# Kernel optimization log

Hardware: AMD Instinct MI355X
Metric: run time of the kernel (lower is better)

The kernel has to match this reference:

```python
import jax, jax.numpy as jnp
import numpy as np

EPS = 1e-5
TEMP = 0.07
LARGE_NEG = -1e9


def mi_net(x, W1, g1, b1, W2, b2, Ws, lng, lnb):
    # x: (B, C, T). 1x1 convs == per-position channel projections.
    y = jnp.einsum('bct,oc->bot', x, W1)                      # conv1 (no bias)
    mu = y.mean(axis=(0, 2), keepdims=True)                   # BatchNorm2d, training-mode batch stats
    var = y.var(axis=(0, 2), keepdims=True)
    y = (y - mu) * jax.lax.rsqrt(var + EPS) * g1[None, :, None] + b1[None, :, None]
    y = jax.nn.relu(y)
    y = jnp.einsum('bot,po->bpt', y, W2) + b2[None, :, None]  # conv2 (bias)
    h = y + jnp.einsum('bct,oc->bot', x, Ws)                  # linear shortcut
    mu2 = h.mean(axis=1, keepdims=True)                       # LayerNorm over channel dim
    v2 = h.var(axis=1, keepdims=True)
    return (h - mu2) * jax.lax.rsqrt(v2 + EPS) * lng[None, :, None] + lnb[None, :, None]


def infonce(L, G):
    # L: (N, D, T) locals, G: (N, D) single global per sample (n_multis = 1)
    N, D, T = L.shape
    l_p = jnp.swapaxes(L, 1, 2)                               # (N, T, D)
    l_p = l_p / jnp.linalg.norm(l_p, axis=2, keepdims=True)
    g = G / jnp.linalg.norm(G, axis=1, keepdims=True)         # (N, D)
    u_p = (jnp.einsum('ntd,nd->nt', l_p, g) / TEMP)[:, :, None]   # (N, T, 1), positives scaled by temp
    # negatives: <global_i, local_{j,t}>; NOT divided by temperature (faithful to torch source)
    u_n = jnp.einsum('nd,mtd->nmt', g, l_p)                   # (N, N, T)
    eye = jnp.eye(N, dtype=bool)[:, :, None]
    u_n = jnp.where(eye, LARGE_NEG, u_n).reshape(N, N * T)    # mask self pairs
    logits = jnp.concatenate(
        [u_p, jnp.broadcast_to(u_n[:, None, :], (N, T, N * T))], axis=2)  # (N, T, 1+N*T)
    logp = jax.nn.log_softmax(logits, axis=2)
    return -logp[:, :, 0].mean()


def setup_inputs() -> dict:
    key = jax.random.key(0)
    ks = jax.random.split(key, 10)
    B, CL, CG, T, MI = 32, 1536, 192, 256, 512
    d = {
        'local_feat': jax.random.normal(ks[0], (B, CL, T), jnp.float32),
        'global_feat': jax.random.normal(ks[1], (B, CG), jnp.float32),
        # local_net params
        'lW1': jax.random.normal(ks[2], (MI, CL), jnp.float32) * 0.02,
        'lg1': jnp.ones((MI,), jnp.float32),
        'lb1': jnp.zeros((MI,), jnp.float32),
        'lW2': jax.random.normal(ks[3], (MI, MI), jnp.float32) * 0.02,
        'lb2': jnp.zeros((MI,), jnp.float32),
        'lWs': jax.random.normal(ks[4], (MI, CL), jnp.float32) * 0.02,
        'llng': jnp.ones((MI,), jnp.float32),
        'llnb': jnp.zeros((MI,), jnp.float32),
        # global_net params (global_channels != mi_units -> net exists)
        'gW1': jax.random.normal(ks[5], (MI, CG), jnp.float32) * 0.02,
        'gg1': jnp.ones((MI,), jnp.float32),
        'gb1': jnp.zeros((MI,), jnp.float32),
        'gW2': jax.random.normal(ks[6], (MI, MI), jnp.float32) * 0.02,
        'gb2': jnp.zeros((MI,), jnp.float32),
    }
    # shortcut with near-identity init (n_units >= n_input for global net)
    gWs = jax.random.uniform(ks[7], (MI, CG), jnp.float32, -0.01, 0.01)
    gWs = gWs.at[jnp.arange(CG), jnp.arange(CG)].set(1.0)
    d['gWs'] = gWs
    d['glng'] = jnp.ones((MI,), jnp.float32)
    d['glnb'] = jnp.zeros((MI,), jnp.float32)
    return d


def reference(local_feat, global_feat,
              lW1, lg1, lb1, lW2, lb2, lWs, llng, llnb,
              gW1, gg1, gb1, gW2, gb2, gWs, glng, glnb):
    L = mi_net(local_feat, lW1, lg1, lb1, lW2, lb2, lWs, llng, llnb)      # (B, MI, T)
    G = mi_net(global_feat[:, :, None], gW1, gg1, gb1, gW2, gb2, gWs, glng, glnb)[:, :, 0]  # (B, MI)
    return infonce(L, G)
```

## Files before the change

kernel.cpp:

```cpp
#include <hip/hip_runtime.h>

#define B 32
#define CL 1536
#define CG 192
#define T 256
#define MI 512
#define NPOS 8192
#define EPS 1e-5f
#define TEMP 0.07f

typedef __attribute__((ext_vector_type(8))) __bf16 bf16x8;
typedef __attribute__((ext_vector_type(4))) float f32x4;

__device__ __forceinline__ unsigned short f2bf(float f) {
  union { float f; unsigned u; } v; v.f = f;
  unsigned r = v.u + 0x7FFFu + ((v.u >> 16) & 1u);
  return (unsigned short)(r >> 16);
}
__device__ __forceinline__ float bf2f(unsigned short h) {
  union { unsigned u; float f; } v; v.u = ((unsigned)h) << 16;
  return v.f;
}

__device__ __forceinline__ float wave_sum(float v) {
#pragma unroll
  for (int off = 32; off > 0; off >>= 1) v += __shfl_xor(v, off, 64);
  return v;
}
__device__ __forceinline__ float block_sum(float v, float* rb) {
  v = wave_sum(v);
  __syncthreads();
  if ((threadIdx.x & 63) == 0) rb[threadIdx.x >> 6] = v;
  __syncthreads();
  return rb[0] + rb[1] + rb[2] + rb[3];
}
__device__ __forceinline__ float bs128(float v, float* rb) {
  v = wave_sum(v);
  __syncthreads();
  if ((threadIdx.x & 63) == 0) rb[threadIdx.x >> 6] = v;
  __syncthreads();
  return rb[0] + rb[1];
}

__global__ __launch_bounds__(256) void k_prep(
    const float* __restrict__ x, const float* __restrict__ lW1,
    const float* __restrict__ lWs, const float* __restrict__ lW2,
    const float* __restrict__ gx, const float* __restrict__ gW1,
    unsigned short* __restrict__ xT, unsigned short* __restrict__ Wc,
    unsigned short* __restrict__ W2b, float* __restrict__ y1g,
    float* __restrict__ bsum) {
  __shared__ float xs[64][65];
  const int bi = blockIdx.x, tid = threadIdx.x;
  if (bi < 1792) {
    int idx = (bi * 256 + tid) * 4;
    const float* src; unsigned short* dst;
    if (idx < 786432) { src = lW1 + idx; dst = Wc + idx; }
    else if (idx < 1572864) { src = lWs + (idx - 786432); dst = Wc + idx; }
    else { src = lW2 + (idx - 1572864); dst = W2b + (idx - 1572864); }
    float4 v = *(const float4*)src;
    ushort4 o = {f2bf(v.x), f2bf(v.y), f2bf(v.z), f2bf(v.w)};
    *(ushort4*)dst = o;
  } else if (bi < 4864) {
    int bi2 = bi - 1792;
    int b = bi2 / 96, rem = bi2 - b * 96;
    int c0 = (rem >> 2) * 64, t0 = (rem & 3) * 64;
    const float* xb = x + ((size_t)b * CL + c0) * T + t0;
#pragma unroll
    for (int i = 0; i < 16; i++) {
      int idx = tid + i * 256, c = idx >> 6, t = idx & 63;
      xs[c][t] = xb[(size_t)c * T + t];
    }
    __syncthreads();
    unsigned short* ob = xT + ((size_t)b * T + t0) * CL + c0;
#pragma unroll
    for (int i = 0; i < 8; i++) {
      int idx = tid + i * 256, t = idx >> 5, k = (idx & 31) * 2;
      ushort2 v = {f2bf(xs[k][t]), f2bf(xs[k + 1][t])};
      *(ushort2*)&ob[(size_t)t * CL + k] = v;
    }
  } else if (bi < 4928) {
    int idx = (bi - 4864) * 256 + tid;
    int b = idx & 31, o = idx >> 5;
    float s = 0.f;
    for (int c = 0; c < CG; c++) s = fmaf(gx[b * CG + c], gW1[o * CG + c], s);
    y1g[o * 32 + b] = s;
  } else {
    float4 z = {0.f, 0.f, 0.f, 0.f};
    ((float4*)bsum)[tid] = z;
  }
}

__global__ __launch_bounds__(128, 4) void k_gemm1(
    const unsigned short* __restrict__ xT, const unsigned short* __restrict__ Wc,
    unsigned short* __restrict__ y1u, unsigned short* __restrict__ ysb,
    float* __restrict__ bsum, float* __restrict__ bsq,
    const float* __restrict__ y1g, const float* __restrict__ gg1,
    const float* __restrict__ gb1, const float* __restrict__ gW2,
    const float* __restrict__ gb2, const float* __restrict__ gx,
    const float* __restrict__ gWsc, float* __restrict__ hg) {
  const int tid = threadIdx.x, bi = blockIdx.x;
  if (bi >= 2048) {
    __shared__ float gsc[512], gsh[512];
#pragma unroll
    for (int jj = 0; jj < 4; jj++) {
      int o = tid + jj * 128;
      float s = 0.f, s2 = 0.f;
      for (int b = 0; b < 32; b++) {
        float v = y1g[o * 32 + b];
        s += v; s2 = fmaf(v, v, s2);
      }
      float mu = s * (1.f / 32.f);
      float var = s2 * (1.f / 32.f) - mu * mu;
      float sc = gg1[o] * rsqrtf(var + EPS);
      gsc[o] = sc;
      gsh[o] = gb1[o] - mu * sc;
    }
    __syncthreads();
    int base = (bi - 2048) * 256;
#pragma unroll
    for (int jj = 0; jj < 2; jj++) {
      int idx = base + jj * 128 + tid;
      int b = idx & 31, p = idx >> 5;
      float s = gb2[p];
      for (int o = 0; o < MI; o++) {
        float v = fmaxf(fmaf(y1g[o * 32 + b], gsc[o], gsh[o]), 0.f);
        s = fmaf(v, gW2[(size_t)p * MI + o], s);
      }
      for (int c = 0; c < CG; c++) s = fmaf(gx[b * CG + c], gWsc[p * CG + c], s);
      hg[p * 32 + b] = s;
    }
    return;
  }
  __shared__ __align__(16) unsigned short As[64][32];
  __shared__ __align__(16) unsigned short Bs[64][32];
  __shared__ float ps[64], pq[64];
  const int w = tid >> 6, lane = tid & 63;
  const int m0 = (bi & 127) * 64, o0 = (bi >> 7) * 64;
  const int sr = lane >> 2, sc = (lane & 3) * 8;
  const int lm = lane & 15, q = lane >> 4;
  f32x4 acc[4][2];
#pragma unroll
  for (int i = 0; i < 4; i++)
#pragma unroll
    for (int j = 0; j < 2; j++) acc[i][j] = f32x4{0.f, 0.f, 0.f, 0.f};

  const unsigned short* pa = xT + (size_t)(m0 + w * 32 + sr) * CL + sc;
  const unsigned short* pb = Wc + (size_t)(o0 + w * 32 + sr) * CL + sc;
  for (int k0 = 0; k0 < CL; k0 += 32) {
    __builtin_amdgcn_global_load_lds(
        (const __attribute__((address_space(1))) void*)(pa + k0),
        (__attribute__((address_space(3))) void*)&As[w * 32][0], 16, 0, 0);
    __builtin_amdgcn_global_load_lds(
        (const __attribute__((address_space(1))) void*)(pa + 16 * CL + k0),
        (__attribute__((address_space(3))) void*)&As[w * 32 + 16][0], 16, 0, 0);
    __builtin_amdgcn_global_load_lds(
        (const __attribute__((address_space(1))) void*)(pb + k0),
        (__attribute__((address_space(3))) void*)&Bs[w * 32][0], 16, 0, 0);
    __builtin_amdgcn_global_load_lds(
        (const __attribute__((address_space(1))) void*)(pb + 16 * CL + k0),
        (__attribute__((address_space(3))) void*)&Bs[w * 32 + 16][0], 16, 0, 0);
    __syncthreads();
    bf16x8 af[4], bfr[2];
#pragma unroll
    for (int mi = 0; mi < 4; mi++)
      af[mi] = *(const bf16x8*)&As[mi * 16 + lm][q * 8];
#pragma unroll
    for (int ni = 0; ni < 2; ni++)
      bfr[ni] = *(const bf16x8*)&Bs[w * 32 + ni * 16 + lm][q * 8];
#pragma unroll
    for (int mi = 0; mi < 4; mi++)
#pragma unroll
      for (int ni = 0; ni < 2; ni++)
        acc[mi][ni] = __builtin_amdgcn_mfma_f32_16x16x32_bf16(
            af[mi], bfr[ni], acc[mi][ni], 0, 0, 0);
    __syncthreads();
  }
  const int row0 = m0 + q * 4;
  const bool isY1 = (o0 < 512);
  unsigned short* dst = isY1 ? y1u : ysb;
  const int ob = isY1 ? o0 : o0 - 512;
#pragma unroll
  for (int mi = 0; mi < 4; mi++)
#pragma unroll
    for (int ni = 0; ni < 2; ni++) {
      int oc = ob + w * 32 + ni * 16 + lm;
#pragma unroll
      for (int r = 0; r < 4; r++)
        dst[(size_t)(row0 + mi * 16 + r) * 512 + oc] = f2bf(acc[mi][ni][r]);
    }
  if (isY1) {
#pragma unroll
    for (int ni = 0; ni < 2; ni++) {
      float s = 0.f, s2 = 0.f;
#pragma unroll
      for (int mi = 0; mi < 4; mi++)
#pragma unroll
        for (int r = 0; r < 4; r++) {
          float v = acc[mi][ni][r];
          s += v; s2 = fmaf(v, v, s2);
        }
      s += __shfl_xor(s, 16, 64);  s2 += __shfl_xor(s2, 16, 64);
      s += __shfl_xor(s, 32, 64);  s2 += __shfl_xor(s2, 32, 64);
      if (q == 0) {
        int c = w * 32 + ni * 16 + lm;
        ps[c] = s; pq[c] = s2;
      }
    }
    __syncthreads();
    if (tid < 64) {
      atomicAdd(&bsum[o0 + tid], ps[tid]);
      atomicAdd(&bsq[o0 + tid], pq[tid]);
    }
  }
}

__global__ __launch_bounds__(256) void k_bnapp(
    const unsigned short* __restrict__ y1u, const float* __restrict__ bsum,
    const float* __restrict__ bsq, const float* __restrict__ lg1,
    const float* __restrict__ lb1, unsigned short* __restrict__ vv) {
  int idx = (blockIdx.x * 256 + threadIdx.x) * 4;
  int o = idx & 511;
  ushort4 in = *(const ushort4*)&y1u[idx];
  float iv[4] = {bf2f(in.x), bf2f(in.y), bf2f(in.z), bf2f(in.w)};
  unsigned short ov[4];
#pragma unroll
  for (int j = 0; j < 4; j++) {
    float mu = bsum[o + j] * (1.f / NPOS);
    float var = bsq[o + j] * (1.f / NPOS) - mu * mu;
    float sc = lg1[o + j] * rsqrtf(var + EPS);
    float sh = lb1[o + j] - mu * sc;
    ov[j] = f2bf(fmaxf(fmaf(iv[j], sc, sh), 0.f));
  }
  ushort4 out = {ov[0], ov[1], ov[2], ov[3]};
  *(ushort4*)&vv[idx] = out;
}

__global__ __launch_bounds__(128, 4) void k_gemm2(
    const unsigned short* __restrict__ vv, const unsigned short* __restrict__ W2b,
    const float* __restrict__ b2, const unsigned short* __restrict__ ysb,
    unsigned short* __restrict__ hb16,
    const float* __restrict__ hg, const float* __restrict__ glng,
    const float* __restrict__ glnb, unsigned short* __restrict__ gnormb) {
  __shared__ __align__(16) unsigned short As[64][32];
  __shared__ __align__(16) unsigned short Bs[64][32];
  __shared__ float rb[2];
  const int tid = threadIdx.x, bi = blockIdx.x;
  if (bi >= 1024) {
    int b = bi - 1024;
    float v[4], Lv[4];
    float s = 0.f, s2 = 0.f;
#pragma unroll
    for (int j = 0; j < 4; j++) {
      v[j] = hg[(tid + j * 128) * 32 + b];
      s += v[j]; s2 = fmaf(v[j], v[j], s2);
    }
    s = bs128(s, rb);
    s2 = bs128(s2, rb);
    float mu = s * (1.f / MI);
    float var = s2 * (1.f / MI) - mu * mu;
    float rstd = rsqrtf(var + EPS);
    float n2 = 0.f;
#pragma unroll
    for (int j = 0; j < 4; j++) {
      int p = tid + j * 128;
      Lv[j] = fmaf((v[j] - mu) * rstd, glng[p], glnb[p]);
      n2 = fmaf(Lv[j], Lv[j], n2);
    }
    n2 = bs128(n2, rb);
    float inv = rsqrtf(n2);
#pragma unroll
    for (int j = 0; j < 4; j++)
      gnormb[b * MI + tid + j * 128] = f2bf(Lv[j] * inv);
    return;
  }
  const int w = tid >> 6, lane = tid & 63;
  const int m0 = (bi & 127) * 64, p0 = (bi >> 7) * 64;
  const int sr = lane >> 2, sc = (lane & 3) * 8;
  const int lm = lane & 15, q = lane >> 4;
  f32x4 acc[4][2];
#pragma unroll
  for (int i = 0; i < 4; i++)
#pragma unroll
    for (int j = 0; j < 2; j++) acc[i][j] = f32x4{0.f, 0.f, 0.f, 0.f};

  const unsigned short* pa = vv + (size_t)(m0 + w * 32 + sr) * 512 + sc;
  const unsigned short* pb = W2b + (size_t)(p0 + w * 32 + sr) * 512 + sc;
  for (int k0 = 0; k0 < 512; k0 += 32) {
    __builtin_amdgcn_global_load_lds(
        (const __attribute__((address_space(1))) void*)(pa + k0),
        (__attribute__((address_space(3))) void*)&As[w * 32][0], 16, 0, 0);
    __builtin_amdgcn_global_load_lds(
        (const __attribute__((address_space(1))) void*)(pa + 16 * 512 + k0),
        (__attribute__((address_space(3))) void*)&As[w * 32 + 16][0], 16, 0, 0);
    __builtin_amdgcn_global_load_lds(
        (const __attribute__((address_space(1))) void*)(pb + k0),
        (__attribute__((address_space(3))) void*)&Bs[w * 32][0], 16, 0, 0);
    __builtin_amdgcn_global_load_lds(
        (const __attribute__((address_space(1))) void*)(pb + 16 * 512 + k0),
        (__attribute__((address_space(3))) void*)&Bs[w * 32 + 16][0], 16, 0, 0);
    __syncthreads();
    bf16x8 af[4], bfr[2];
#pragma unroll
    for (int mi = 0; mi < 4; mi++)
      af[mi] = *(const bf16x8*)&As[mi * 16 + lm][q * 8];
#pragma unroll
    for (int ni = 0; ni < 2; ni++)
      bfr[ni] = *(const bf16x8*)&Bs[w * 32 + ni * 16 + lm][q * 8];
#pragma unroll
    for (int mi = 0; mi < 4; mi++)
#pragma unroll
      for (int ni = 0; ni < 2; ni++)
        acc[mi][ni] = __builtin_amdgcn_mfma_f32_16x16x32_bf16(
            af[mi], bfr[ni], acc[mi][ni], 0, 0, 0);
    __syncthreads();
  }
  const int row0 = m0 + q * 4;
#pragma unroll
  for (int ni = 0; ni < 2; ni++) {
    int p = p0 + w * 32 + ni * 16 + lm;
    float bias = b2[p];
#pragma unroll
    for (int mi = 0; mi < 4; mi++)
#pragma unroll
      for (int r = 0; r < 4; r++) {
        size_t off = (size_t)(row0 + mi * 16 + r) * 512 + p;
        hb16[off] = f2bf(acc[mi][ni][r] + bias + bf2f(ysb[off]));
      }
  }
}

__global__ __launch_bounds__(256) void k_tail(
    const unsigned short* __restrict__ hb16, const float* __restrict__ lng,
    const float* __restrict__ lnb, const unsigned short* __restrict__ gnormb,
    float* __restrict__ up, float* __restrict__ pmax, float* __restrict__ psum) {
  __shared__ __align__(16) unsigned short gs[32 * 512];
  __shared__ __align__(16) unsigned short Ls[32 * 512];
  __shared__ float Ured[4 * 1024];
  const int tid = threadIdx.x;
  const int w = tid >> 6, lane = tid & 63;
  const int r0 = blockIdx.x * 32;
  const int smp = r0 >> 8;
#pragma unroll
  for (int i = 0; i < 8; i++) {
    int e = (tid + i * 256) * 8;
    *(uint4*)&gs[e] = *(const uint4*)&gnormb[e];
  }
  float4 g0 = *(const float4*)&lng[lane * 8];
  float4 g1 = *(const float4*)&lng[lane * 8 + 4];
  float4 bb0 = *(const float4*)&lnb[lane * 8];
  float4 bb1 = *(const float4*)&lnb[lane * 8 + 4];
  float gg[8] = {g0.x, g0.y, g0.z, g0.w, g1.x, g1.y, g1.z, g1.w};
  float bz[8] = {bb0.x, bb0.y, bb0.z, bb0.w, bb1.x, bb1.y, bb1.z, bb1.w};
#pragma unroll
  for (int j = 0; j < 8; j++) {
    int rr = w * 8 + j;
    const unsigned short* row = hb16 + (size_t)(r0 + rr) * 512 + lane * 8;
    ushort4 u0 = *(const ushort4*)row;
    ushort4 u1 = *(const ushort4*)(row + 4);
    float v[8] = {bf2f(u0.x), bf2f(u0.y), bf2f(u0.z), bf2f(u0.w),
                  bf2f(u1.x), bf2f(u1.y), bf2f(u1.z), bf2f(u1.w)};
    float s = 0.f, s2 = 0.f;
#pragma unroll
    for (int k = 0; k < 8; k++) { s += v[k]; s2 = fmaf(v[k], v[k], s2); }
    s = wave_sum(s);
    s2 = wave_sum(s2);
    float mu = s * (1.f / MI);
    float var = s2 * (1.f / MI) - mu * mu;
    float rstd = rsqrtf(var + EPS);
    float L[8], n2 = 0.f;
#pragma unroll
    for (int k = 0; k < 8; k++) {
      L[k] = fmaf((v[k] - mu) * rstd, gg[k], bz[k]);
      n2 = fmaf(L[k], L[k], n2);
    }
    n2 = wave_sum(n2);
    float inv = rsqrtf(n2);
    unsigned short* orow = &Ls[rr * 512 + lane * 8];
    ushort4 o0 = {f2bf(L[0] * inv), f2bf(L[1] * inv), f2bf(L[2] * inv), f2bf(L[3] * inv)};
    ushort4 o1 = {f2bf(L[4] * inv), f2bf(L[5] * inv), f2bf(L[6] * inv), f2bf(L[7] * inv)};
    *(ushort4*)orow = o0;
    *(ushort4*)(orow + 4) = o1;
  }
  __syncthreads();
  const int lm = lane & 15, q = lane >> 4;
  f32x4 acc[2][2];
#pragma unroll
  for (int i = 0; i < 2; i++)
#pragma unroll
    for (int j = 0; j < 2; j++) acc[i][j] = f32x4{0.f, 0.f, 0.f, 0.f};
#pragma unroll
  for (int kk = 0; kk < 4; kk++) {
    int k0 = w * 128 + kk * 32 + q * 8;
    bf16x8 af[2], bfr[2];
#pragma unroll
    for (int mi = 0; mi < 2; mi++)
      af[mi] = *(const bf16x8*)&gs[(mi * 16 + lm) * 512 + k0];
#pragma unroll
    for (int ni = 0; ni < 2; ni++)
      bfr[ni] = *(const bf16x8*)&Ls[(ni * 16 + lm) * 512 + k0];
#pragma unroll
    for (int mi = 0; mi < 2; mi++)
#pragma unroll
      for (int ni = 0; ni < 2; ni++)
        acc[mi][ni] = __builtin_amdgcn_mfma_f32_16x16x32_bf16(
            af[mi], bfr[ni], acc[mi][ni], 0, 0, 0);
  }
#pragma unroll
  for (int mi = 0; mi < 2; mi++)
#pragma unroll
    for (int ni = 0; ni < 2; ni++)
#pragma unroll
      for (int r = 0; r < 4; r++) {
        int m = mi * 16 + q * 4 + r, n = ni * 16 + lm;
        Ured[w * 1024 + m * 32 + n] = acc[mi][ni][r];
      }
  __syncthreads();
  float u[4];
#pragma unroll
  for (int j = 0; j < 4; j++) {
    int idx = tid * 4 + j;
    u[j] = Ured[idx] + Ured[1024 + idx] + Ured[2048 + idx] + Ured[3072 + idx];
  }
  __syncthreads();
#pragma unroll
  for (int j = 0; j < 4; j++) Ured[tid * 4 + j] = u[j];
  int m = (tid * 4) >> 5;
  if (m == smp) {
#pragma unroll
    for (int j = 0; j < 4; j++)
      up[r0 + ((tid * 4 + j) & 31)] = u[j] * (1.f / TEMP);
  }
  __syncthreads();
  if (tid < 32) {
    float mx = -1e30f, s = 0.f;
    if (tid != smp) {
      for (int n = 0; n < 32; n++) mx = fmaxf(mx, Ured[tid * 32 + n]);
      for (int n = 0; n < 32; n++) s += expf(Ured[tid * 32 + n] - mx);
    }
    pmax[tid * 256 + blockIdx.x] = mx;
    psum[tid * 256 + blockIdx.x] = s;
  }
}

__global__ __launch_bounds__(256) void k_loss(
    const float* __restrict__ up, const float* __restrict__ pmax,
    const float* __restrict__ psum, float* __restrict__ out) {
  __shared__ float rb[4];
  __shared__ float red[32][8];
  __shared__ float Ms[32], Ss[32];
  const int tid = threadIdx.x;
  const int n = tid >> 3, j = tid & 7;
  float mx = -1e30f;
  for (int c = j * 32; c < j * 32 + 32; c++) mx = fmaxf(mx, pmax[n * 256 + c]);
  red[n][j] = mx;
  __syncthreads();
  if (j == 0) {
    float M = -1e30f;
#pragma unroll
    for (int k = 0; k < 8; k++) M = fmaxf(M, red[n][k]);
    Ms[n] = M;
  }
  __syncthreads();
  float M = Ms[n];
  float s = 0.f;
  for (int c = j * 32; c < j * 32 + 32; c++)
    s += psum[n * 256 + c] * expf(pmax[n * 256 + c] - M);
  __syncthreads();
  red[n][j] = s;
  __syncthreads();
  if (j == 0) {
    float S = 0.f;
#pragma unroll
    for (int k = 0; k < 8; k++) S += red[n][k];
    Ss[n] = S;
  }
  __syncthreads();
  float acc = 0.f;
  for (int i = tid; i < NPOS; i += 256) {
    int nn = i >> 8;
    float upv = up[i];
    float Mn = Ms[nn], Sn = Ss[nn];
    float mx2 = fmaxf(upv, Mn);
    float lse = mx2 + logf(expf(upv - mx2) + Sn * expf(Mn - mx2));
    acc += lse - upv;
  }
  acc = block_sum(acc, rb);
  if (tid == 0) out[0] = acc * (1.f / NPOS);
}

extern "C" void kernel_launch(void* const* d_in, const int* in_sizes, int n_in,
                              void* d_out, int out_size, void* d_ws, size_t ws_size,
                              hipStream_t stream) {
  (void)in_sizes; (void)n_in; (void)out_size; (void)ws_size;
  const float* x    = (const float*)d_in[0];
  const float* gx   = (const float*)d_in[1];
  const float* lW1  = (const float*)d_in[2];
  const float* lg1  = (const float*)d_in[3];
  const float* lb1  = (const float*)d_in[4];
  const float* lW2  = (const float*)d_in[5];
  const float* lb2  = (const float*)d_in[6];
  const float* lWs  = (const float*)d_in[7];
  const float* llng = (const float*)d_in[8];
  const float* llnb = (const float*)d_in[9];
  const float* gW1  = (const float*)d_in[10];
  const float* gg1  = (const float*)d_in[11];
  const float* gb1  = (const float*)d_in[12];
  const float* gW2  = (const float*)d_in[13];
  const float* gb2  = (const float*)d_in[14];
  const float* gWs  = (const float*)d_in[15];
  const float* glng = (const float*)d_in[16];
  const float* glnb = (const float*)d_in[17];

  char* wsb = (char*)d_ws;
  unsigned short* xT     = (unsigned short*)(wsb);
  unsigned short* Wc     = (unsigned short*)(wsb + 25165824);
  unsigned short* W2b    = (unsigned short*)(wsb + 28311552);
  unsigned short* y1u    = (unsigned short*)(wsb + 28835840);
  unsigned short* ysb    = (unsigned short*)(wsb + 37224448);
  unsigned short* vv     = (unsigned short*)(wsb + 45613056);
  unsigned short* hb16   = (unsigned short*)(wsb + 54001664);
  float* bsum            = (float*)(wsb + 71827456);
  float* bsq             = (float*)(wsb + 71829504);
  float* y1g             = (float*)(wsb + 71831552);
  float* hg              = (float*)(wsb + 71901184);
  unsigned short* gnormb = (unsigned short*)(wsb + 71966720);
  float* up              = (float*)(wsb + 71999488);
  float* pmax            = (float*)(wsb + 72032256);
  float* psum            = (float*)(wsb + 72065024);

  k_prep<<<dim3(4929), 256, 0, stream>>>(x, lW1, lWs, lW2, gx, gW1, xT, Wc, W2b,
                                         y1g, bsum);
  k_gemm1<<<dim3(2112), 128, 0, stream>>>(xT, Wc, y1u, ysb, bsum, bsq,
                                          y1g, gg1, gb1, gW2, gb2, gx, gWs, hg);
  k_bnapp<<<dim3(4096), 256, 0, stream>>>(y1u, bsum, bsq, lg1, lb1, vv);
  k_gemm2<<<dim3(1056), 128, 0, stream>>>(vv, W2b, lb2, ysb, hb16,
                                          hg, glng, glnb, gnormb);
  k_tail<<<dim3(256), 256, 0, stream>>>(hb16, llng, llnb, gnormb, up, pmax, psum);
  k_loss<<<dim3(1), 256, 0, stream>>>(up, pmax, psum, (float*)d_out);
}
```

Measured before the change: 254.2 us.

## Enlarge GEMM tiles to 128x128, move shortcut add into tail, relocate global LN

Both bf16 MFMA GEMMs go from 64x64 tiles with 128 threads to 128x128 tiles with 256 threads laid out as a 2x2 wave grid. This doubles operand reuse per LDS load and cuts global traffic, at the cost of far fewer blocks (256 for gemm2) and more accumulator registers. The shortcut add (ysb) moves from the gemm2 epilogue into k_tail, and the global-feature LayerNorm moves from gemm2 into k_bnapp. The x transpose in k_prep now writes 16-byte packed stores, and BN stat atomics are issued directly from each wave instead of going through shared memory.

```diff
diff --git a/kernel.cpp b/kernel.cpp
--- a/kernel.cpp
+++ b/kernel.cpp
@@ -33,13 +33,6 @@
   if ((threadIdx.x & 63) == 0) rb[threadIdx.x >> 6] = v;
   __syncthreads();
   return rb[0] + rb[1] + rb[2] + rb[3];
-}
-__device__ __forceinline__ float bs128(float v, float* rb) {
-  v = wave_sum(v);
-  __syncthreads();
-  if ((threadIdx.x & 63) == 0) rb[threadIdx.x >> 6] = v;
-  __syncthreads();
-  return rb[0] + rb[1];
 }
 
 __global__ __launch_bounds__(256) void k_prep(
@@ -73,10 +66,17 @@
     __syncthreads();
     unsigned short* ob = xT + ((size_t)b * T + t0) * CL + c0;
 #pragma unroll
-    for (int i = 0; i < 8; i++) {
-      int idx = tid + i * 256, t = idx >> 5, k = (idx & 31) * 2;
-      ushort2 v = {f2bf(xs[k][t]), f2bf(xs[k + 1][t])};
-      *(ushort2*)&ob[(size_t)t * CL + k] = v;
+    for (int half = 0; half < 2; half++) {
+      int s = tid + half * 256;
+      int t = s >> 3, kg = s & 7;
+      unsigned short v[8];
+#pragma unroll
+      for (int j = 0; j < 8; j++) v[j] = f2bf(xs[kg * 8 + j][t]);
+      uint4 o = {(unsigned)v[0] | ((unsigned)v[1] << 16),
+                 (unsigned)v[2] | ((unsigned)v[3] << 16),
+                 (unsigned)v[4] | ((unsigned)v[5] << 16),
+                 (unsigned)v[6] | ((unsigned)v[7] << 16)};
+      *(uint4*)&ob[(size_t)t * CL + kg * 8] = o;
     }
   } else if (bi < 4928) {
     int idx = (bi - 4864) * 256 + tid;
@@ -90,7 +90,7 @@
   }
 }
 
-__global__ __launch_bounds__(128, 4) void k_gemm1(
+__global__ __launch_bounds__(256, 2) void k_gemm1(
     const unsigned short* __restrict__ xT, const unsigned short* __restrict__ Wc,
     unsigned short* __restrict__ y1u, unsigned short* __restrict__ ysb,
     float* __restrict__ bsum, float* __restrict__ bsq,
@@ -99,11 +99,11 @@
     const float* __restrict__ gb2, const float* __restrict__ gx,
     const float* __restrict__ gWsc, float* __restrict__ hg) {
   const int tid = threadIdx.x, bi = blockIdx.x;
-  if (bi >= 2048) {
+  if (bi >= 512) {
     __shared__ float gsc[512], gsh[512];
 #pragma unroll
-    for (int jj = 0; jj < 4; jj++) {
-      int o = tid + jj * 128;
+    for (int jj = 0; jj < 2; jj++) {
+      int o = tid + jj * 256;
       float s = 0.f, s2 = 0.f;
       for (int b = 0; b < 32; b++) {
         float v = y1g[o * 32 + b];
@@ -116,81 +116,79 @@
       gsh[o] = gb1[o] - mu * sc;
     }
     __syncthreads();
-    int base = (bi - 2048) * 256;
-#pragma unroll
-    for (int jj = 0; jj < 2; jj++) {
-      int idx = base + jj * 128 + tid;
-      int b = idx & 31, p = idx >> 5;
-      float s = gb2[p];
-      for (int o = 0; o < MI; o++) {
-        float v = fmaxf(fmaf(y1g[o * 32 + b], gsc[o], gsh[o]), 0.f);
-        s = fmaf(v, gW2[(size_t)p * MI + o], s);
-      }
-      for (int c = 0; c < CG; c++) s = fmaf(gx[b * CG + c], gWsc[p * CG + c], s);
-      hg[p * 32 + b] = s;
-    }
+    int idx = (bi - 512) * 256 + tid;
+    int b = idx & 31, p = idx >> 5;
+    float s = gb2[p];
+    for (int o = 0; o < MI; o++) {
+      float v = fmaxf(fmaf(y1g[o * 32 + b], gsc[o], gsh[o]), 0.f);
+      s = fmaf(v, gW2[(size_t)p * MI + o], s);
+    }
+    for (int c = 0; c < CG; c++) s = fmaf(gx[b * CG + c], gWsc[p * CG + c], s);
+    hg[p * 32 + b] = s;
     return;
   }
-  __shared__ __align__(16) unsigned short As[64][32];
-  __shared__ __align__(16) unsigned short Bs[64][32];
-  __shared__ float ps[64], pq[64];
+  __shared__ __align__(16) unsigned short As[128][32];
+  __shared__ __align__(16) unsigned short Bs[128][32];
   const int w = tid >> 6, lane = tid & 63;
-  const int m0 = (bi & 127) * 64, o0 = (bi >> 7) * 64;
+  const int m0 = (bi & 63) * 128, o0 = (bi >> 6) * 128;
   const int sr = lane >> 2, sc = (lane & 3) * 8;
+  const int wm = w & 1, wn = w >> 1;
   const int lm = lane & 15, q = lane >> 4;
-  f32x4 acc[4][2];
+  f32x4 acc[4][4];
 #pragma unroll
   for (int i = 0; i < 4; i++)
 #pragma unroll
-    for (int j = 0; j < 2; j++) acc[i][j] = f32x4{0.f, 0.f, 0.f, 0.f};
-
-  const unsigned short* pa = xT + (size_t)(m0 + w * 32 + sr) * CL + sc;
-  const unsigned short* pb = Wc + (size_t)(o0 + w * 32 + sr) * CL + sc;
-  for (int k0 = 0; k0 < CL; k0 += 32) {
-    __builtin_amdgcn_global_load_lds(
-        (const __attribute__((address_space(1))) void*)(pa + k0),
+    for (int j = 0; j < 4; j++) acc[i][j] = f32x4{0.f, 0.f, 0.f, 0.f};
+
+  const unsigned short* pa0 = xT + (size_t)(m0 + w * 32 + sr) * CL + sc;
+  const unsigned short* pa1 = pa0 + (size_t)16 * CL;
+  const unsigned short* pb0 = Wc + (size_t)(o0 + w * 32 + sr) * CL + sc;
+  const unsigned short* pb1 = pb0 + (size_t)16 * CL;
+  for (int c0 = 0; c0 < CL; c0 += 32) {
+    __builtin_amdgcn_global_load_lds(
+        (const __attribute__((address_space(1))) void*)(pa0 + c0),
         (__attribute__((address_space(3))) void*)&As[w * 32][0], 16, 0, 0);
     __builtin_amdgcn_global_load_lds(
-        (const __attribute__((address_space(1))) void*)(pa + 16 * CL + k0),
+        (const __attribute__((address_space(1))) void*)(pa1 + c0),
         (__attribute__((address_space(3))) void*)&As[w * 32 + 16][0], 16, 0, 0);
     __builtin_amdgcn_global_load_lds(
-        (const __attribute__((address_space(1))) void*)(pb + k0),
+        (const __attribute__((address_space(1))) void*)(pb0 + c0),
         (__attribute__((address_space(3))) void*)&Bs[w * 32][0], 16, 0, 0);
     __builtin_amdgcn_global_load_lds(
-        (const __attribute__((address_space(1))) void*)(pb + 16 * CL + k0),
+        (const __attribute__((address_space(1))) void*)(pb1 + c0),
         (__attribute__((address_space(3))) void*)&Bs[w * 32 + 16][0], 16, 0, 0);
     __syncthreads();
-    bf16x8 af[4], bfr[2];
+    bf16x8 af[4], bfr[4];
 #pragma unroll
     for (int mi = 0; mi < 4; mi++)
-      af[mi] = *(const bf16x8*)&As[mi * 16 + lm][q * 8];
-#pragma unroll
-    for (int ni = 0; ni < 2; ni++)
-      bfr[ni] = *(const bf16x8*)&Bs[w * 32 + ni * 16 + lm][q * 8];
+      af[mi] = *(const bf16x8*)&As[wm * 64 + mi * 16 + lm][q * 8];
+#pragma unroll
+    for (int ni = 0; ni < 4; ni++)
+      bfr[ni] = *(const bf16x8*)&Bs[wn * 64 + ni * 16 + lm][q * 8];
 #pragma unroll
     for (int mi = 0; mi < 4; mi++)
 #pragma unroll
-      for (int ni = 0; ni < 2; ni++)
+      for (int ni = 0; ni < 4; ni++)
         acc[mi][ni] = __builtin_amdgcn_mfma_f32_16x16x32_bf16(
             af[mi], bfr[ni], acc[mi][ni], 0, 0, 0);
     __syncthreads();
   }
-  const int row0 = m0 + q * 4;
+  const int row0 = m0 + wm * 64 + q * 4;
   const bool isY1 = (o0 < 512);
   unsigned short* dst = isY1 ? y1u : ysb;
   const int ob = isY1 ? o0 : o0 - 512;
 #pragma unroll
   for (int mi = 0; mi < 4; mi++)
 #pragma unroll
-    for (int ni = 0; ni < 2; ni++) {
-      int oc = ob + w * 32 + ni * 16 + lm;
+    for (int ni = 0; ni < 4; ni++) {
+      int oc = ob + wn * 64 + ni * 16 + lm;
 #pragma unroll
       for (int r = 0; r < 4; r++)
         dst[(size_t)(row0 + mi * 16 + r) * 512 + oc] = f2bf(acc[mi][ni][r]);
     }
   if (isY1) {
 #pragma unroll
-    for (int ni = 0; ni < 2; ni++) {
+    for (int ni = 0; ni < 4; ni++) {
       float s = 0.f, s2 = 0.f;
 #pragma unroll
       for (int mi = 0; mi < 4; mi++)
@@ -202,14 +200,10 @@
       s += __shfl_xor(s, 16, 64);  s2 += __shfl_xor(s2, 16, 64);
       s += __shfl_xor(s, 32, 64);  s2 += __shfl_xor(s2, 32, 64);
       if (q == 0) {
-        int c = w * 32 + ni * 16 + lm;
-        ps[c] = s; pq[c] = s2;
+        int c = o0 + wn * 64 + ni * 16 + lm;
+        atomicAdd(&bsum[c], s);
+        atomicAdd(&bsq[c], s2);
       }
-    }
-    __syncthreads();
-    if (tid < 64) {
-      atomicAdd(&bsum[o0 + tid], ps[tid]);
-      atomicAdd(&bsq[o0 + tid], pq[tid]);
     }
   }
 }
@@ -217,8 +211,29 @@
 __global__ __launch_bounds__(256) void k_bnapp(
     const unsigned short* __restrict__ y1u, const float* __restrict__ bsum,
     const float* __restrict__ bsq, const float* __restrict__ lg1,
-    const float* __restrict__ lb1, unsigned short* __restrict__ vv) {
-  int idx = (blockIdx.x * 256 + threadIdx.x) * 4;
+    const float* __restrict__ lb1, unsigned short* __restrict__ vv,
+    const float* __restrict__ hg, const float* __restrict__ glng,
+    const float* __restrict__ glnb, unsigned short* __restrict__ gnormb) {
+  __shared__ float rb[4];
+  const int bi = blockIdx.x, tid = threadIdx.x;
+  if (bi >= 4096) {
+    int b = bi - 4096;
+    float v0 = hg[tid * 32 + b];
+    float v1 = hg[(tid + 256) * 32 + b];
+    float s = block_sum(v0 + v1, rb);
+    float s2 = block_sum(fmaf(v0, v0, v1 * v1), rb);
+    float mu = s * (1.f / MI);
+    float var = s2 * (1.f / MI) - mu * mu;
+    float rstd = rsqrtf(var + EPS);
+    float L0 = fmaf((v0 - mu) * rstd, glng[tid], glnb[tid]);
+    float L1 = fmaf((v1 - mu) * rstd, glng[tid + 256], glnb[tid + 256]);
+    float n2 = block_sum(fmaf(L0, L0, L1 * L1), rb);
+    float inv = rsqrtf(n2);
+    gnormb[b * MI + tid] = f2bf(L0 * inv);
+    gnormb[b * MI + tid + 256] = f2bf(L1 * inv);
+    return;
+  }
+  int idx = (bi * 256 + tid) * 4;
   int o = idx & 511;
   ushort4 in = *(const ushort4*)&y1u[idx];
   float iv[4] = {bf2f(in.x), bf2f(in.y), bf2f(in.z), bf2f(in.w)};
@@ -235,103 +250,75 @@
   *(ushort4*)&vv[idx] = out;
 }
 
-__global__ __launch_bounds__(128, 4) void k_gemm2(
+__global__ __launch_bounds__(256, 2) void k_gemm2(
     const unsigned short* __restrict__ vv, const unsigned short* __restrict__ W2b,
-    const float* __restrict__ b2, const unsigned short* __restrict__ ysb,
-    unsigned short* __restrict__ hb16,
-    const float* __restrict__ hg, const float* __restrict__ glng,
-    const float* __restrict__ glnb, unsigned short* __restrict__ gnormb) {
-  __shared__ __align__(16) unsigned short As[64][32];
-  __shared__ __align__(16) unsigned short Bs[64][32];
-  __shared__ float rb[2];
+    const float* __restrict__ b2, unsigned short* __restrict__ hb16) {
+  __shared__ __align__(16) unsigned short As[128][32];
+  __shared__ __align__(16) unsigned short Bs[128][32];
   const int tid = threadIdx.x, bi = blockIdx.x;
-  if (bi >= 1024) {
-    int b = bi - 1024;
-    float v[4], Lv[4];
-    float s = 0.f, s2 = 0.f;
-#pragma unroll
-    for (int j = 0; j < 4; j++) {
-      v[j] = hg[(tid + j * 128) * 32 + b];
-      s += v[j]; s2 = fmaf(v[j], v[j], s2);
-    }
-    s = bs128(s, rb);
-    s2 = bs128(s2, rb);
-    float mu = s * (1.f / MI);
-    float var = s2 * (1.f / MI) - mu * mu;
-    float rstd = rsqrtf(var + EPS);
-    float n2 = 0.f;
-#pragma unroll
-    for (int j = 0; j < 4; j++) {
-      int p = tid + j * 128;
-      Lv[j] = fmaf((v[j] - mu) * rstd, glng[p], glnb[p]);
-      n2 = fmaf(Lv[j], Lv[j], n2);
-    }
-    n2 = bs128(n2, rb);
-    float inv = rsqrtf(n2);
-#pragma unroll
-    for (int j = 0; j < 4; j++)
-      gnormb[b * MI + tid + j * 128] = f2bf(Lv[j] * inv);
-    return;
-  }
   const int w = tid >> 6, lane = tid & 63;
-  const int m0 = (bi & 127) * 64, p0 = (bi >> 7) * 64;
+  const int m0 = (bi & 63) * 128, p0 = (bi >> 6) * 128;
   const int sr = lane >> 2, sc = (lane & 3) * 8;
+  const int wm = w & 1, wn = w >> 1;
   const int lm = lane & 15, q = lane >> 4;
-  f32x4 acc[4][2];
+  f32x4 acc[4][4];
 #pragma unroll
   for (int i = 0; i < 4; i++)
 #pragma unroll
-    for (int j = 0; j < 2; j++) acc[i][j] = f32x4{0.f, 0.f, 0.f, 0.f};
-
-  const unsigned short* pa = vv + (size_t)(m0 + w * 32 + sr) * 512 + sc;
-  const unsigned short* pb = W2b + (size_t)(p0 + w * 32 + sr) * 512 + sc;
-  for (int k0 = 0; k0 < 512; k0 += 32) {
-    __builtin_amdgcn_global_load_lds(
-        (const __attribute__((address_space(1))) void*)(pa + k0),
+    for (int j = 0; j < 4; j++) acc[i][j] = f32x4{0.f, 0.f, 0.f, 0.f};
+
+  const unsigned short* pa0 = vv + (size_t)(m0 + w * 32 + sr) * 512 + sc;
+  const unsigned short* pa1 = pa0 + (size_t)16 * 512;
+  const unsigned short* pb0 = W2b + (size_t)(p0 + w * 32 + sr) * 512 + sc;
+  const unsigned short* pb1 = pb0 + (size_t)16 * 512;
+  for (int c0 = 0; c0 < 512; c0 += 32) {
+    __builtin_amdgcn_global_load_lds(
+        (const __attribute__((address_space(1))) void*)(pa0 + c0),
         (__attribute__((address_space(3))) void*)&As[w * 32][0], 16, 0, 0);
     __builtin_amdgcn_global_load_lds(
-        (const __attribute__((address_space(1))) void*)(pa + 16 * 512 + k0),
+        (const __attribute__((address_space(1))) void*)(pa1 + c0),
         (__attribute__((address_space(3))) void*)&As[w * 32 + 16][0], 16, 0, 0);
     __builtin_amdgcn_global_load_lds(
-        (const __attribute__((address_space(1))) void*)(pb + k0),
+        (const __attribute__((address_space(1))) void*)(pb0 + c0),
         (__attribute__((address_space(3))) void*)&Bs[w * 32][0], 16, 0, 0);
     __builtin_amdgcn_global_load_lds(
-        (const __attribute__((address_space(1))) void*)(pb + 16 * 512 + k0),
+        (const __attribute__((address_space(1))) void*)(pb1 + c0),
         (__attribute__((address_space(3))) void*)&Bs[w * 32 + 16][0], 16, 0, 0);
     __syncthreads();
-    bf16x8 af[4], bfr[2];
+    bf16x8 af[4], bfr[4];
 #pragma unroll
     for (int mi = 0; mi < 4; mi++)
-      af[mi] = *(const bf16x8*)&As[mi * 16 + lm][q * 8];
-#pragma unroll
-    for (int ni = 0; ni < 2; ni++)
-      bfr[ni] = *(const bf16x8*)&Bs[w * 32 + ni * 16 + lm][q * 8];
+      af[mi] = *(const bf16x8*)&As[wm * 64 + mi * 16 + lm][q * 8];
+#pragma unroll
+    for (int ni = 0; ni < 4; ni++)
+      bfr[ni] = *(const bf16x8*)&Bs[wn * 64 + ni * 16 + lm][q * 8];
 #pragma unroll
     for (int mi = 0; mi < 4; mi++)
 #pragma unroll
-      for (int ni = 0; ni < 2; ni++)
+      for (int ni = 0; ni < 4; ni++)
         acc[mi][ni] = __builtin_amdgcn_mfma_f32_16x16x32_bf16(
             af[mi], bfr[ni], acc[mi][ni], 0, 0, 0);
     __syncthreads();
   }
-  const int row0 = m0 + q * 4;
-#pragma unroll
-  for (int ni = 0; ni < 2; ni++) {
-    int p = p0 + w * 32 + ni * 16 + lm;
+  const int row0 = m0 + wm * 64 + q * 4;
+#pragma unroll
+  for (int ni = 0; ni < 4; ni++) {
+    int p = p0 + wn * 64 + ni * 16 + lm;
     float bias = b2[p];
 #pragma unroll
     for (int mi = 0; mi < 4; mi++)
 #pragma unroll
       for (int r = 0; r < 4; r++) {
         size_t off = (size_t)(row0 + mi * 16 + r) * 512 + p;
-        hb16[off] = f2bf(acc[mi][ni][r] + bias + bf2f(ysb[off]));
+        hb16[off] = f2bf(acc[mi][ni][r] + bias);
       }
   }
 }
 
 __global__ __launch_bounds__(256) void k_tail(
-    const unsigned short* __restrict__ hb16, const float* __restrict__ lng,
-    const float* __restrict__ lnb, const unsigned short* __restrict__ gnormb,
+    const unsigned short* __restrict__ hb16, const unsigned short* __restrict__ ysb,
+    const float* __restrict__ lng, const float* __restrict__ lnb,
+    const unsigned short* __restrict__ gnormb,
     float* __restrict__ up, float* __restrict__ pmax, float* __restrict__ psum) {
   __shared__ __align__(16) unsigned short gs[32 * 512];
   __shared__ __align__(16) unsigned short Ls[32 * 512];
@@ -354,14 +341,26 @@
 #pragma unroll
   for (int j = 0; j < 8; j++) {
     int rr = w * 8 + j;
-    const unsigned short* row = hb16 + (size_t)(r0 + rr) * 512 + lane * 8;
-    ushort4 u0 = *(const ushort4*)row;
-    ushort4 u1 = *(const ushort4*)(row + 4);
-    float v[8] = {bf2f(u0.x), bf2f(u0.y), bf2f(u0.z), bf2f(u0.w),
-                  bf2f(u1.x), bf2f(u1.y), bf2f(u1.z), bf2f(u1.w)};
+    size_t off = (size_t)(r0 + rr) * 512 + lane * 8;
+    uint4 hu = *(const uint4*)&hb16[off];
+    uint4 yu = *(const uint4*)&ysb[off];
+    unsigned short hv[8] = {
+        (unsigned short)(hu.x & 0xffff), (unsigned short)(hu.x >> 16),
+        (unsigned short)(hu.y & 0xffff), (unsigned short)(hu.y >> 16),
+        (unsigned short)(hu.z & 0xffff), (unsigned short)(hu.z >> 16),
+        (unsigned short)(hu.w & 0xffff), (unsigned short)(hu.w >> 16)};
+    unsigned short yv[8] = {
+        (unsigned short)(yu.x & 0xffff), (unsigned short)(yu.x >> 16),
+        (unsigned short)(yu.y & 0xffff), (unsigned short)(yu.y >> 16),
+        (unsigned short)(yu.z & 0xffff), (unsigned short)(yu.z >> 16),
+        (unsigned short)(yu.w & 0xffff), (unsigned short)(yu.w >> 16)};
+    float v[8];
     float s = 0.f, s2 = 0.f;
 #pragma unroll
-    for (int k = 0; k < 8; k++) { s += v[k]; s2 = fmaf(v[k], v[k], s2); }
+    for (int k = 0; k < 8; k++) {
+      v[k] = bf2f(hv[k]) + bf2f(yv[k]);
+      s += v[k]; s2 = fmaf(v[k], v[k], s2);
+    }
     s = wave_sum(s);
     s2 = wave_sum(s2);
     float mu = s * (1.f / MI);
@@ -519,22 +518,23 @@
   unsigned short* ysb    = (unsigned short*)(wsb + 37224448);
   unsigned short* vv     = (unsigned short*)(wsb + 45613056);
   unsigned short* hb16   = (unsigned short*)(wsb + 54001664);
-  float* bsum            = (float*)(wsb + 71827456);
-  float* bsq             = (float*)(wsb + 71829504);
-  float* y1g             = (float*)(wsb + 71831552);
-  float* hg              = (float*)(wsb + 71901184);
-  unsigned short* gnormb = (unsigned short*)(wsb + 71966720);
-  float* up              = (float*)(wsb + 71999488);
-  float* pmax            = (float*)(wsb + 72032256);
-  float* psum            = (float*)(wsb + 72065024);
+  float* bsum            = (float*)(wsb + 62390272);
+  float* bsq             = (float*)(wsb + 62392320);
+  float* y1g             = (float*)(wsb + 62394368);
+  float* hg              = (float*)(wsb + 62459904);
+  unsigned short* gnormb = (unsigned short*)(wsb + 62525440);
+  float* up              = (float*)(wsb + 62558208);
+  float* pmax            = (float*)(wsb + 62590976);
+  float* psum            = (float*)(wsb + 62623744);
 
   k_prep<<<dim3(4929), 256, 0, stream>>>(x, lW1, lWs, lW2, gx, gW1, xT, Wc, W2b,
                                          y1g, bsum);
-  k_gemm1<<<dim3(2112), 128, 0, stream>>>(xT, Wc, y1u, ysb, bsum, bsq,
-                                          y1g, gg1, gb1, gW2, gb2, gx, gWs, hg);
-  k_bnapp<<<dim3(4096), 256, 0, stream>>>(y1u, bsum, bsq, lg1, lb1, vv);
-  k_gemm2<<<dim3(1056), 128, 0, stream>>>(vv, W2b, lb2, ysb, hb16,
+  k_gemm1<<<dim3(576), 256, 0, stream>>>(xT, Wc, y1u, ysb, bsum, bsq,
+                                         y1g, gg1, gb1, gW2, gb2, gx, gWs, hg);
+  k_bnapp<<<dim3(4128), 256, 0, stream>>>(y1u, bsum, bsq, lg1, lb1, vv,
                                           hg, glng, glnb, gnormb);
-  k_tail<<<dim3(256), 256, 0, stream>>>(hb16, llng, llnb, gnormb, up, pmax, psum);
+  k_gemm2<<<dim3(256), 256, 0, stream>>>(vv, W2b, lb2, hb16);
+  k_tail<<<dim3(256), 256, 0, stream>>>(hb16, ysb, llng, llnb, gnormb,
+                                        up, pmax, psum);
   k_loss<<<dim3(1), 256, 0, stream>>>(up, pmax, psum, (float*)d_out);
 }
```

After: 219.1 us. 1.16x faster.
